# Kernel tuning notes

Hardware: AMD Instinct MI355X
Metric: run time of the kernel (lower is better)

The kernel has to match this reference:

```python
import jax, jax.numpy as jnp
import numpy as np

# --- Instant-NGP hash-grid constants (from __init__ defaults) ---
T = 2 ** 19          # hash table size per level
NLEVELS = 16
F = 2                # features per level
L = 4                # dir positional-encoding frequencies
LEVELS = np.geomspace(16, 2048, NLEVELS, dtype=int)            # grid resolutions
PRIMES = jnp.array([1, 2654435761, 805459861], dtype=jnp.uint32)
FREQS = (2.0 ** np.arange(L)).astype(np.float32)
# corner c in 0..7 -> bit b_i = use ceil along dim i (matches torch corner order)
BITS = jnp.array([[(c >> i) & 1 for i in range(3)] for c in range(8)], dtype=bool)  # (8,3)


def _hash_encode(pos, table):
    """pos: (P,3) level-scaled positions; table: (T,F). Returns (P,F).
    Spatial hash + gather + trilinear interpolation (== grid_sample trick)."""
    fl = jnp.floor(pos)
    ce = jnp.ceil(pos)
    frac = pos - fl                                             # (P,3) in [0,1)
    corners = jnp.where(BITS[None], ce[:, None, :], fl[:, None, :]).astype(jnp.int32)  # (P,8,3)
    # uint32 wrap-around arithmetic matches torch int64 mod 2^19 (T is a power of 2)
    v = corners.astype(jnp.uint32) * PRIMES                     # (P,8,3)
    h = (v[..., 0] ^ v[..., 1] ^ v[..., 2]) & jnp.uint32(T - 1) # (P,8)
    cf = table[h]                                               # (P,8,F) irregular gather
    w = jnp.prod(jnp.where(BITS[None], frac[:, None, :], 1.0 - frac[:, None, :]), axis=-1)  # (P,8)
    return jnp.einsum('pc,pcf->pf', w, cf)


def setup_inputs() -> dict:
    key = jax.random.key(0)
    ks = jax.random.split(key, 16)
    N, S = 2048, 192
    # positions s.t. x*scene_scale + 0.5 lies mostly in (0,1), a few outside (mask path)
    x = (jax.random.uniform(ks[0], (N, S, 3), jnp.float32) - 0.5) * 1.1
    r_dir = jax.random.normal(ks[1], (N, S, 3), jnp.float32)
    tables = jax.random.normal(ks[2], (NLEVELS, T, F), jnp.float32) * 1e-4

    def lin(k, fan_in, fan_out):
        return jax.random.normal(k, (fan_in, fan_out), jnp.float32) / np.float32(np.sqrt(fan_in))

    din = F * NLEVELS              # 32
    cin = 16 + 3 + 3 * L * 2       # 43
    return {
        'x': x, 'r_dir': r_dir, 'tables': tables,
        'dW1': lin(ks[3], din, 64), 'db1': jnp.zeros((64,), jnp.float32),
        'dW2': lin(ks[4], 64, 16), 'db2': jnp.zeros((16,), jnp.float32),
        'cW1': lin(ks[5], cin, 64), 'cb1': jnp.zeros((64,), jnp.float32),
        'cW2': lin(ks[6], 64, 64), 'cb2': jnp.zeros((64,), jnp.float32),
        'cW3': lin(ks[7], 64, 3), 'cb3': jnp.zeros((3,), jnp.float32),
    }


def reference(x, r_dir, tables, dW1, db1, dW2, db2, cW1, cb1, cW2, cb2, cW3, cb3):
    scene_scale = 1.0
    N, S = x.shape[0], r_dir.shape[1]
    xf = x.reshape(-1, 3) * scene_scale + 0.5          # (P,3)
    rd = r_dir.reshape(-1, 3)                          # (P,3)
    mask = jnp.all(xf > 0, axis=-1) & jnp.all(xf < 1, axis=-1)  # (P,)

    # multi-resolution hash encoding (fixed 16-level loop, vectorized over points)
    feats = jnp.concatenate(
        [_hash_encode(xf * np.float32(LEVELS[i]), tables[i]) for i in range(NLEVELS)],
        axis=-1)                                       # (P, F*NLEVELS)

    log_sigma = jax.nn.relu(feats @ dW1 + db1) @ dW2 + db2        # (P,16)

    # direction positional encoding: [dir, sin(2^l*2pi*dir), cos(...)] -> (P, 3+3*2L)
    xin = rd[..., None] * (2.0 * np.pi * jnp.asarray(FREQS))      # (P,3,L)
    enc = jnp.concatenate([jnp.sin(xin), jnp.cos(xin)], axis=-1).reshape(rd.shape[0], -1)
    enc_dir = jnp.concatenate([rd, enc], axis=-1)                 # (P,27)

    h = jax.nn.relu(jnp.concatenate([log_sigma, enc_dir], axis=-1) @ cW1 + cb1)
    h = jax.nn.relu(h @ cW2 + cb2)
    color = jax.nn.sigmoid(h @ cW3 + cb3)                         # (P,3)

    color = jnp.where(mask[:, None], color, 0.0)
    sigma = jnp.where(mask[:, None], jnp.exp(log_sigma[:, :1]), 0.0)
    return color.reshape(N, S, 3), sigma.reshape(N, S, 1)
```

## Files before the change

### kernel.cpp

```cpp
#include <hip/hip_runtime.h>
#include <hip/hip_bf16.h>
#include <cstdint>

#define NPTS (2048 * 192)
#define TBL  (1u << 19)
#define TMASK (TBL - 1u)
#define PBLOCKS (NPTS / 256)
#define ENC_BLOCKS (PBLOCKS * 16)
#define PREP_BLOCKS 6
#define PE_BLOCKS PBLOCKS
#define MLP_BLOCKS 3072
#define P2 2654435761u
#define P3 805459861u

__constant__ float LVLS[16] = {16.f, 22.f, 30.f, 42.f, 58.f, 80.f, 111.f, 153.f,
                               212.f, 294.f, 406.f, 561.f, 776.f, 1072.f, 1482.f, 2048.f};

__device__ __forceinline__ uint32_t f2bf(float f) {
    uint32_t u = __float_as_uint(f);
    return (u + 0x7FFFu + ((u >> 16) & 1u)) >> 16;
}
__device__ __forceinline__ uint32_t pack2(float a, float b) {
    return f2bf(a) | (f2bf(b) << 16);
}
__device__ __forceinline__ uint32_t pack2t(float a, float b) {
    return __builtin_amdgcn_perm(__float_as_uint(b), __float_as_uint(a),
                                 0x07060302u);
}

#if __has_builtin(__builtin_amdgcn_sinf)
#define SIN_REV(x) __builtin_amdgcn_sinf(x)
#else
#define SIN_REV(x) __sinf(6.28318530717958647f * (x))
#endif

typedef __attribute__((ext_vector_type(8))) short bf16x8;
typedef __attribute__((ext_vector_type(4))) float f32x4;

#define MFMA_BF16 __builtin_amdgcn_mfma_f32_16x16x32_bf16

__device__ __forceinline__ float pe_val(int r, float rx, float ry, float rz)
{
    int t = r - 19;
    int d = t >> 3;
    int s = t & 7;
    float comp = (d == 0) ? rx : ((d == 1) ? ry : rz);
    float a = ldexpf(comp, s & 3) + ((s >= 4) ? 0.25f : 0.0f);
    float v = SIN_REV(a);
    if (r == 16) v = rx;
    if (r == 17) v = ry;
    if (r == 18) v = rz;
    if (r == 43) v = 1.0f;
    if (r > 43)  v = 0.0f;
    return v;
}

__global__ __launch_bounds__(256) void k_encode(const float* __restrict__ x,
                                                const float* __restrict__ tables,
                                                uint32_t* __restrict__ feats,
                                                const float* __restrict__ dW1,
                                                const float* __restrict__ dW2,
                                                const float* __restrict__ cW1,
                                                const float* __restrict__ cb1,
                                                const float* __restrict__ cW2,
                                                const float* __restrict__ cW3,
                                                uint4* __restrict__ wfrags,
                                                const float* __restrict__ rdir,
                                                uint32_t* __restrict__ dirs)
{
    if (blockIdx.x >= ENC_BLOCKS + PREP_BLOCKS) {
        int p = (blockIdx.x - ENC_BLOCKS - PREP_BLOCKS) * 256 + threadIdx.x;
        size_t p3 = (size_t)p * 3;
        float rx = rdir[p3 + 0], ry = rdir[p3 + 1], rz = rdir[p3 + 2];
#pragma unroll
        for (int i = 0; i < 14; ++i)
            dirs[(size_t)i * NPTS + p] =
                pack2t(pe_val(16 + 2 * i, rx, ry, rz),
                       pe_val(17 + 2 * i, rx, ry, rz));
        return;
    }
    if (blockIdx.x >= ENC_BLOCKS) {
        int t = (blockIdx.x - ENC_BLOCKS) * 256 + threadIdx.x;
        if (t >= 24 * 64) return;
        int frag = t >> 6, lane = t & 63;
        const float* W; const float* bfold = nullptr;
        int OUT, Kact, Mact, k0, m0;
        if (frag < 4)       { W = dW1; OUT = 64; Kact = 32; Mact = 64; k0 = 0;               m0 = frag * 16; }
        else if (frag < 6)  { W = dW2; OUT = 16; Kact = 64; Mact = 16; k0 = (frag - 4) * 32; m0 = 0; }
        else if (frag < 14) { int i = frag - 6;  W = cW1; OUT = 64; Kact = 43; Mact = 64;
                              k0 = (i & 1) * 32; m0 = (i >> 1) * 16; bfold = cb1; }
        else if (frag < 22) { int i = frag - 14; W = cW2; OUT = 64; Kact = 64; Mact = 64;
                              k0 = (i & 1) * 32; m0 = (i >> 1) * 16; }
        else                { W = cW3; OUT = 3;  Kact = 64; Mact = 3;  k0 = (frag - 22) * 32; m0 = 0; }
        int m  = m0 + (lane & 15);
        int kq = k0 + ((lane >> 4) << 3);
        uint32_t d[4];
#pragma unroll
        for (int j = 0; j < 4; ++j) {
            float a0 = 0.f, a1 = 0.f;
            int ka = kq + 2 * j, kb = ka + 1;
            if (m < Mact) {
                a0 = (ka < Kact) ? W[(size_t)ka * OUT + m]
                                 : ((bfold && ka == Kact) ? bfold[m] : 0.f);
                a1 = (kb < Kact) ? W[(size_t)kb * OUT + m]
                                 : ((bfold && kb == Kact) ? bfold[m] : 0.f);
            }
            d[j] = f2bf(a0) | (f2bf(a1) << 16);
        }
        wfrags[t] = make_uint4(d[0], d[1], d[2], d[3]);
        return;
    }

    int xs   = blockIdx.x & 7;
    int i    = blockIdx.x >> 3;
    int half = i / PBLOCKS;
    int pb   = i - half * PBLOCKS;
    int lvl  = xs + (half << 3);
    int p    = pb * 256 + threadIdx.x;

    size_t p3 = (size_t)p * 3;
    float x0 = x[p3 + 0] + 0.5f;
    float x1 = x[p3 + 1] + 0.5f;
    float x2 = x[p3 + 2] + 0.5f;
    size_t oidx = (size_t)lvl * NPTS + p;

    bool m = (x0 > 0.f) && (x0 < 1.f) && (x1 > 0.f) && (x1 < 1.f) &&
             (x2 > 0.f) && (x2 < 1.f);
    if (!m) { feats[oidx] = 0u; return; }

    float s  = LVLS[lvl];
    float px = x0 * s, py = x1 * s, pz = x2 * s;
    float flx = floorf(px), fly = floorf(py), flz = floorf(pz);
    float frx = px - flx,   fry = py - fly,   frz = pz - flz;
    int ix = (int)flx, iy = (int)fly, iz = (int)flz;
    uint32_t ux = (uint32_t)ix, uy = (uint32_t)iy, uz = (uint32_t)iz;

    uint32_t base[4];
    base[0] = (uy * P2) ^ (uz * P3);
    base[1] = ((uy + 1u) * P2) ^ (uz * P3);
    base[2] = (uy * P2) ^ ((uz + 1u) * P3);
    base[3] = ((uy + 1u) * P2) ^ ((uz + 1u) * P3);

    const float2* tb = (const float2*)tables + (size_t)lvl * TBL;

    float2 v[8];
    if ((ix & 1) == 0) {
        const float4* tb4 = (const float4*)tb;
#pragma unroll
        for (int cc = 0; cc < 4; ++cc) {
            uint32_t h0 = (base[cc] ^ ux) & TMASK;
            float4 qv = tb4[h0 >> 1];
            bool hi = (h0 & 1u) != 0u;
            float2 e0 = hi ? make_float2(qv.z, qv.w) : make_float2(qv.x, qv.y);
            float2 e1 = hi ? make_float2(qv.x, qv.y) : make_float2(qv.z, qv.w);
            v[(cc << 1)]     = e0;
            v[(cc << 1) | 1] = e1;
        }
    } else {
        uint32_t h[8];
#pragma unroll
        for (int c = 0; c < 8; ++c)
            h[c] = (base[c >> 1] ^ (ux + (uint32_t)(c & 1))) & TMASK;
#pragma unroll
        for (int c = 0; c < 8; ++c) v[c] = tb[h[c]];
    }

    float f0 = 0.f, f1 = 0.f;
#pragma unroll
    for (int c = 0; c < 8; ++c) {
        float w = ((c & 1)        ? frx : 1.f - frx)
                * (((c >> 1) & 1) ? fry : 1.f - fry)
                * (((c >> 2) & 1) ? frz : 1.f - frz);
        f0 += w * v[c].x;
        f1 += w * v[c].y;
    }
    feats[oidx] = pack2(f0, f1);
}

__device__ __forceinline__ bf16x8 trans_frag(uint32_t p01a, uint32_t p23a,
                                             uint32_t p01b, uint32_t p23b, int lane)
{
    int q = lane >> 4, col = lane & 15;
    int srcA = (((q & 1) << 1) << 4) | col;
    int srcB = srcA + 16;
    uint32_t a0 = (uint32_t)__shfl((int)p01a, srcA, 64);
    uint32_t b0 = (uint32_t)__shfl((int)p01b, srcA, 64);
    uint32_t a1 = (uint32_t)__shfl((int)p23a, srcA, 64);
    uint32_t b1 = (uint32_t)__shfl((int)p23b, srcA, 64);
    uint32_t a2 = (uint32_t)__shfl((int)p01a, srcB, 64);
    uint32_t b2 = (uint32_t)__shfl((int)p01b, srcB, 64);
    uint32_t a3 = (uint32_t)__shfl((int)p23a, srcB, 64);
    uint32_t b3 = (uint32_t)__shfl((int)p23b, srcB, 64);
    bool hi = q >= 2;
    union { bf16x8 v; uint32_t d[4]; } u;
    u.d[0] = hi ? b0 : a0;
    u.d[1] = hi ? b1 : a1;
    u.d[2] = hi ? b2 : a2;
    u.d[3] = hi ? b3 : a3;
    return u.v;
}

__global__ __launch_bounds__(256, 4) void k_mlp(const uint32_t* __restrict__ feats,
                                                const uint4* __restrict__ wfrags,
                                                const float* __restrict__ x,
                                                const uint32_t* __restrict__ dirs,
                                                const float* __restrict__ db1,
                                                const float* __restrict__ db2,
                                                const float* __restrict__ cb2,
                                                const float* __restrict__ cb3,
                                                float* __restrict__ out)
{
    __shared__ uint4 wlds[24 * 64];
#pragma unroll
    for (int t = 0; t < 6; ++t)
        wlds[t * 256 + threadIdx.x] = wfrags[t * 256 + threadIdx.x];
    __syncthreads();

    int lane = threadIdx.x & 63;
    int q = lane >> 4, col = lane & 15;
    int wgid = blockIdx.x * 4 + (threadIdx.x >> 6);

#define LDW(f) ({ union { uint4 u_; bf16x8 v_; } w_; w_.u_ = wlds[(f) * 64 + lane]; w_.v_; })

#pragma unroll
    for (int it = 0; it < 2; ++it) {
        int g = (wgid * 2 + it) << 4;
        int pt = g + col;
        size_t pt3 = (size_t)pt * 3;

        union { bf16x8 v; uint32_t d[4]; } Bf;
#pragma unroll
        for (int w = 0; w < 4; ++w)
            Bf.d[w] = feats[(size_t)(q * 4 + w) * NPTS + g + col];

        uint32_t da[4], dbv[4];
#pragma unroll
        for (int j = 0; j < 4; ++j) {
            int pa = ((q - 2) * 4 + j) & 7;
            da[j] = dirs[(size_t)pa * NPTS + pt];
            int pb = 8 + q * 4 + j;
            pb = (pb > 13) ? 13 : pb;
            dbv[j] = dirs[(size_t)pb * NPTS + pt];
        }

        f32x4 T[4];
#pragma unroll
        for (int mt = 0; mt < 4; ++mt) {
            const float4 bb = *(const float4*)&db1[mt * 16 + q * 4];
            f32x4 c; c[0] = bb.x; c[1] = bb.y; c[2] = bb.z; c[3] = bb.w;
            T[mt] = MFMA_BF16(LDW(mt), Bf.v, c, 0, 0, 0);
        }
        uint32_t p01[4], p23[4];
#pragma unroll
        for (int mt = 0; mt < 4; ++mt) {
            p01[mt] = pack2t(fmaxf(T[mt][0], 0.f), fmaxf(T[mt][1], 0.f));
            p23[mt] = pack2t(fmaxf(T[mt][2], 0.f), fmaxf(T[mt][3], 0.f));
        }
        bf16x8 Bh0 = trans_frag(p01[0], p23[0], p01[1], p23[1], lane);
        bf16x8 Bh1 = trans_frag(p01[2], p23[2], p01[3], p23[3], lane);

        f32x4 Dls;
        {
            const float4 bb = *(const float4*)&db2[q * 4];
            f32x4 c; c[0] = bb.x; c[1] = bb.y; c[2] = bb.z; c[3] = bb.w;
            Dls = MFMA_BF16(LDW(4), Bh0, c, 0, 0, 0);
            Dls = MFMA_BF16(LDW(5), Bh1, Dls, 0, 0, 0);
        }
        uint32_t lp01 = pack2t(Dls[0], Dls[1]);
        uint32_t lp23 = pack2t(Dls[2], Dls[3]);

        union { bf16x8 v; uint32_t d[4]; } Ba0, Ba1;
        Ba0.v = trans_frag(lp01, lp23, lp01, lp23, lane);
#pragma unroll
        for (int j = 0; j < 4; ++j) {
            Ba0.d[j] = (q >= 2) ? da[j] : Ba0.d[j];
            bool vld = (q == 0) | ((q == 1) & (j < 2));
            Ba1.d[j] = vld ? dbv[j] : 0u;
        }

        f32x4 C1[4];
#pragma unroll
        for (int mt = 0; mt < 4; ++mt) {
            f32x4 c = {0.f, 0.f, 0.f, 0.f};
            c = MFMA_BF16(LDW(6 + 2 * mt), Ba0.v, c, 0, 0, 0);
            C1[mt] = MFMA_BF16(LDW(7 + 2 * mt), Ba1.v, c, 0, 0, 0);
        }
#pragma unroll
        for (int mt = 0; mt < 4; ++mt) {
            p01[mt] = pack2t(fmaxf(C1[mt][0], 0.f), fmaxf(C1[mt][1], 0.f));
            p23[mt] = pack2t(fmaxf(C1[mt][2], 0.f), fmaxf(C1[mt][3], 0.f));
        }
        bf16x8 Bc0 = trans_frag(p01[0], p23[0], p01[1], p23[1], lane);
        bf16x8 Bc1 = trans_frag(p01[2], p23[2], p01[3], p23[3], lane);

        f32x4 C2[4];
#pragma unroll
        for (int mt = 0; mt < 4; ++mt) {
            const float4 bb = *(const float4*)&cb2[mt * 16 + q * 4];
            f32x4 c; c[0] = bb.x; c[1] = bb.y; c[2] = bb.z; c[3] = bb.w;
            c = MFMA_BF16(LDW(14 + 2 * mt), Bc0, c, 0, 0, 0);
            C2[mt] = MFMA_BF16(LDW(15 + 2 * mt), Bc1, c, 0, 0, 0);
        }
#pragma unroll
        for (int mt = 0; mt < 4; ++mt) {
            p01[mt] = pack2t(fmaxf(C2[mt][0], 0.f), fmaxf(C2[mt][1], 0.f));
            p23[mt] = pack2t(fmaxf(C2[mt][2], 0.f), fmaxf(C2[mt][3], 0.f));
        }
        bf16x8 Bd0 = trans_frag(p01[0], p23[0], p01[1], p23[1], lane);
        bf16x8 Bd1 = trans_frag(p01[2], p23[2], p01[3], p23[3], lane);

        f32x4 c5 = {0.f, 0.f, 0.f, 0.f};
        if (q == 0) { c5[0] = cb3[0]; c5[1] = cb3[1]; c5[2] = cb3[2]; }
        f32x4 Dc = MFMA_BF16(LDW(22), Bd0, c5, 0, 0, 0);
        Dc = MFMA_BF16(LDW(23), Bd1, Dc, 0, 0, 0);

        if (q == 0) {
            float xfx = x[pt3 + 0] + 0.5f;
            float xfy = x[pt3 + 1] + 0.5f;
            float xfz = x[pt3 + 2] + 0.5f;
            bool m = (xfx > 0.f) && (xfx < 1.f) && (xfy > 0.f) && (xfy < 1.f) &&
                     (xfz > 0.f) && (xfz < 1.f);
            out[pt3 + 0] = m ? 1.f / (1.f + __expf(-Dc[0])) : 0.f;
            out[pt3 + 1] = m ? 1.f / (1.f + __expf(-Dc[1])) : 0.f;
            out[pt3 + 2] = m ? 1.f / (1.f + __expf(-Dc[2])) : 0.f;
            out[(size_t)3 * NPTS + pt] = m ? __expf(Dls[0]) : 0.f;
        }
    }
#undef LDW
}

extern "C" void kernel_launch(void* const* d_in, const int* in_sizes, int n_in,
                              void* d_out, int out_size, void* d_ws, size_t ws_size,
                              hipStream_t stream) {
    const float* x      = (const float*)d_in[0];
    const float* rdir   = (const float*)d_in[1];
    const float* tables = (const float*)d_in[2];
    const float* dW1 = (const float*)d_in[3];
    const float* db1 = (const float*)d_in[4];
    const float* dW2 = (const float*)d_in[5];
    const float* db2 = (const float*)d_in[6];
    const float* cW1 = (const float*)d_in[7];
    const float* cb1 = (const float*)d_in[8];
    const float* cW2 = (const float*)d_in[9];
    const float* cb2 = (const float*)d_in[10];
    const float* cW3 = (const float*)d_in[11];
    const float* cb3 = (const float*)d_in[12];
    float* out = (float*)d_out;

    uint4*    wfrags = (uint4*)d_ws;
    uint32_t* feats  = (uint32_t*)((char*)d_ws + 32768);
    uint32_t* dirs   = (uint32_t*)((char*)d_ws + 32768 + (size_t)16 * NPTS * 4);

    k_encode<<<ENC_BLOCKS + PREP_BLOCKS + PE_BLOCKS, 256, 0, stream>>>(
        x, tables, feats, dW1, dW2, cW1, cb1, cW2, cW3, wfrags, rdir, dirs);
    k_mlp<<<MLP_BLOCKS, 256, 0, stream>>>(feats, wfrags, x, dirs,
                                          db1, db2, cb2, cb3, out);
}
```

Baseline: 244.0 us.

## Split hash encode into two level-half launches, use permlane swaps, hoist MLP biases

The single encode launch becomes two: levels 0-7 plus the weight-fragment prep and direction encoding, then levels 8-15. The stated aim is to keep each half's hash-table working set more cache-friendly and to shrink the grid, at the cost of an extra launch. In the MLP, the 64-lane shuffle transposes are replaced with v_permlane32_swap/v_permlane16_swap sequences, which should avoid ds_bpermute traffic through LDS. Bias vectors are also loaded once before the loop instead of on every iteration, which raises register pressure.

```diff
diff --git a/kernel.cpp b/kernel.cpp
--- a/kernel.cpp
+++ b/kernel.cpp
@@ -6,7 +6,7 @@
 #define TBL  (1u << 19)
 #define TMASK (TBL - 1u)
 #define PBLOCKS (NPTS / 256)
-#define ENC_BLOCKS (PBLOCKS * 16)
+#define HALF_BLOCKS (PBLOCKS * 8)
 #define PREP_BLOCKS 6
 #define PE_BLOCKS PBLOCKS
 #define MLP_BLOCKS 3072
@@ -66,21 +66,23 @@
                                                 const float* __restrict__ cW3,
                                                 uint4* __restrict__ wfrags,
                                                 const float* __restrict__ rdir,
-                                                uint32_t* __restrict__ dirs)
-{
-    if (blockIdx.x >= ENC_BLOCKS + PREP_BLOCKS) {
-        int p = (blockIdx.x - ENC_BLOCKS - PREP_BLOCKS) * 256 + threadIdx.x;
-        size_t p3 = (size_t)p * 3;
-        float rx = rdir[p3 + 0], ry = rdir[p3 + 1], rz = rdir[p3 + 2];
-#pragma unroll
-        for (int i = 0; i < 14; ++i)
-            dirs[(size_t)i * NPTS + p] =
-                pack2t(pe_val(16 + 2 * i, rx, ry, rz),
-                       pe_val(17 + 2 * i, rx, ry, rz));
-        return;
-    }
-    if (blockIdx.x >= ENC_BLOCKS) {
-        int t = (blockIdx.x - ENC_BLOCKS) * 256 + threadIdx.x;
+                                                uint32_t* __restrict__ dirs,
+                                                int lvl_base)
+{
+    if (blockIdx.x >= HALF_BLOCKS) {
+        int tb = blockIdx.x - HALF_BLOCKS;
+        if (tb >= PREP_BLOCKS) {
+            int p = (tb - PREP_BLOCKS) * 256 + threadIdx.x;
+            size_t p3 = (size_t)p * 3;
+            float rx = rdir[p3 + 0], ry = rdir[p3 + 1], rz = rdir[p3 + 2];
+#pragma unroll
+            for (int i = 0; i < 14; ++i)
+                dirs[(size_t)i * NPTS + p] =
+                    pack2t(pe_val(16 + 2 * i, rx, ry, rz),
+                           pe_val(17 + 2 * i, rx, ry, rz));
+            return;
+        }
+        int t = tb * 256 + threadIdx.x;
         if (t >= 24 * 64) return;
         int frag = t >> 6, lane = t & 63;
         const float* W; const float* bfold = nullptr;
@@ -112,10 +114,8 @@
     }
 
     int xs   = blockIdx.x & 7;
-    int i    = blockIdx.x >> 3;
-    int half = i / PBLOCKS;
-    int pb   = i - half * PBLOCKS;
-    int lvl  = xs + (half << 3);
+    int pb   = blockIdx.x >> 3;
+    int lvl  = xs + lvl_base;
     int p    = pb * 256 + threadIdx.x;
 
     size_t p3 = (size_t)p * 3;
@@ -177,26 +177,40 @@
     feats[oidx] = pack2(f0, f1);
 }
 
+__device__ __forceinline__ void quad_gather(uint32_t x, uint32_t& e02, uint32_t& e13)
+{
+    uint32_t u = x, v = x;
+    asm("v_permlane32_swap_b32 %0, %1" : "+v"(u), "+v"(v));
+    asm("v_permlane16_swap_b32 %0, %1" : "+v"(u), "+v"(v));
+    e02 = u; e13 = v;
+}
+
 __device__ __forceinline__ bf16x8 trans_frag(uint32_t p01a, uint32_t p23a,
-                                             uint32_t p01b, uint32_t p23b, int lane)
-{
-    int q = lane >> 4, col = lane & 15;
-    int srcA = (((q & 1) << 1) << 4) | col;
-    int srcB = srcA + 16;
-    uint32_t a0 = (uint32_t)__shfl((int)p01a, srcA, 64);
-    uint32_t b0 = (uint32_t)__shfl((int)p01b, srcA, 64);
-    uint32_t a1 = (uint32_t)__shfl((int)p23a, srcA, 64);
-    uint32_t b1 = (uint32_t)__shfl((int)p23b, srcA, 64);
-    uint32_t a2 = (uint32_t)__shfl((int)p01a, srcB, 64);
-    uint32_t b2 = (uint32_t)__shfl((int)p01b, srcB, 64);
-    uint32_t a3 = (uint32_t)__shfl((int)p23a, srcB, 64);
-    uint32_t b3 = (uint32_t)__shfl((int)p23b, srcB, 64);
-    bool hi = q >= 2;
+                                             uint32_t p01b, uint32_t p23b, bool hi)
+{
+    uint32_t a02, a13, c02, c13, b02, b13, e02, e13;
+    quad_gather(p01a, a02, a13);
+    quad_gather(p23a, c02, c13);
+    quad_gather(p01b, b02, b13);
+    quad_gather(p23b, e02, e13);
     union { bf16x8 v; uint32_t d[4]; } u;
-    u.d[0] = hi ? b0 : a0;
-    u.d[1] = hi ? b1 : a1;
-    u.d[2] = hi ? b2 : a2;
-    u.d[3] = hi ? b3 : a3;
+    u.d[0] = hi ? b02 : a02;
+    u.d[1] = hi ? e02 : c02;
+    u.d[2] = hi ? b13 : a13;
+    u.d[3] = hi ? e13 : c13;
+    return u.v;
+}
+
+__device__ __forceinline__ bf16x8 trans_frag1(uint32_t p01, uint32_t p23)
+{
+    uint32_t a02, a13, c02, c13;
+    quad_gather(p01, a02, a13);
+    quad_gather(p23, c02, c13);
+    union { bf16x8 v; uint32_t d[4]; } u;
+    u.d[0] = a02;
+    u.d[1] = c02;
+    u.d[2] = a13;
+    u.d[3] = c13;
     return u.v;
 }
 
@@ -214,11 +228,22 @@
 #pragma unroll
     for (int t = 0; t < 6; ++t)
         wlds[t * 256 + threadIdx.x] = wfrags[t * 256 + threadIdx.x];
-    __syncthreads();
 
     int lane = threadIdx.x & 63;
     int q = lane >> 4, col = lane & 15;
+    bool hi = q >= 2;
     int wgid = blockIdx.x * 4 + (threadIdx.x >> 6);
+
+    float4 b1v[4], c2v[4];
+#pragma unroll
+    for (int mt = 0; mt < 4; ++mt) {
+        b1v[mt] = *(const float4*)&db1[mt * 16 + q * 4];
+        c2v[mt] = *(const float4*)&cb2[mt * 16 + q * 4];
+    }
+    float4 b2v = *(const float4*)&db2[q * 4];
+    float cb30 = cb3[0], cb31 = cb3[1], cb32 = cb3[2];
+
+    __syncthreads();
 
 #define LDW(f) ({ union { uint4 u_; bf16x8 v_; } w_; w_.u_ = wlds[(f) * 64 + lane]; w_.v_; })
 
@@ -246,8 +271,7 @@
         f32x4 T[4];
 #pragma unroll
         for (int mt = 0; mt < 4; ++mt) {
-            const float4 bb = *(const float4*)&db1[mt * 16 + q * 4];
-            f32x4 c; c[0] = bb.x; c[1] = bb.y; c[2] = bb.z; c[3] = bb.w;
+            f32x4 c; c[0] = b1v[mt].x; c[1] = b1v[mt].y; c[2] = b1v[mt].z; c[3] = b1v[mt].w;
             T[mt] = MFMA_BF16(LDW(mt), Bf.v, c, 0, 0, 0);
         }
         uint32_t p01[4], p23[4];
@@ -256,13 +280,12 @@
             p01[mt] = pack2t(fmaxf(T[mt][0], 0.f), fmaxf(T[mt][1], 0.f));
             p23[mt] = pack2t(fmaxf(T[mt][2], 0.f), fmaxf(T[mt][3], 0.f));
         }
-        bf16x8 Bh0 = trans_frag(p01[0], p23[0], p01[1], p23[1], lane);
-        bf16x8 Bh1 = trans_frag(p01[2], p23[2], p01[3], p23[3], lane);
+        bf16x8 Bh0 = trans_frag(p01[0], p23[0], p01[1], p23[1], hi);
+        bf16x8 Bh1 = trans_frag(p01[2], p23[2], p01[3], p23[3], hi);
 
         f32x4 Dls;
         {
-            const float4 bb = *(const float4*)&db2[q * 4];
-            f32x4 c; c[0] = bb.x; c[1] = bb.y; c[2] = bb.z; c[3] = bb.w;
+            f32x4 c; c[0] = b2v.x; c[1] = b2v.y; c[2] = b2v.z; c[3] = b2v.w;
             Dls = MFMA_BF16(LDW(4), Bh0, c, 0, 0, 0);
             Dls = MFMA_BF16(LDW(5), Bh1, Dls, 0, 0, 0);
         }
@@ -270,7 +293,7 @@
         uint32_t lp23 = pack2t(Dls[2], Dls[3]);
 
         union { bf16x8 v; uint32_t d[4]; } Ba0, Ba1;
-        Ba0.v = trans_frag(lp01, lp23, lp01, lp23, lane);
+        Ba0.v = trans_frag1(lp01, lp23);
 #pragma unroll
         for (int j = 0; j < 4; ++j) {
             Ba0.d[j] = (q >= 2) ? da[j] : Ba0.d[j];
@@ -290,14 +313,13 @@
             p01[mt] = pack2t(fmaxf(C1[mt][0], 0.f), fmaxf(C1[mt][1], 0.f));
             p23[mt] = pack2t(fmaxf(C1[mt][2], 0.f), fmaxf(C1[mt][3], 0.f));
         }
-        bf16x8 Bc0 = trans_frag(p01[0], p23[0], p01[1], p23[1], lane);
-        bf16x8 Bc1 = trans_frag(p01[2], p23[2], p01[3], p23[3], lane);
+        bf16x8 Bc0 = trans_frag(p01[0], p23[0], p01[1], p23[1], hi);
+        bf16x8 Bc1 = trans_frag(p01[2], p23[2], p01[3], p23[3], hi);
 
         f32x4 C2[4];
 #pragma unroll
         for (int mt = 0; mt < 4; ++mt) {
-            const float4 bb = *(const float4*)&cb2[mt * 16 + q * 4];
-            f32x4 c; c[0] = bb.x; c[1] = bb.y; c[2] = bb.z; c[3] = bb.w;
+            f32x4 c; c[0] = c2v[mt].x; c[1] = c2v[mt].y; c[2] = c2v[mt].z; c[3] = c2v[mt].w;
             c = MFMA_BF16(LDW(14 + 2 * mt), Bc0, c, 0, 0, 0);
             C2[mt] = MFMA_BF16(LDW(15 + 2 * mt), Bc1, c, 0, 0, 0);
         }
@@ -306,11 +328,11 @@
             p01[mt] = pack2t(fmaxf(C2[mt][0], 0.f), fmaxf(C2[mt][1], 0.f));
             p23[mt] = pack2t(fmaxf(C2[mt][2], 0.f), fmaxf(C2[mt][3], 0.f));
         }
-        bf16x8 Bd0 = trans_frag(p01[0], p23[0], p01[1], p23[1], lane);
-        bf16x8 Bd1 = trans_frag(p01[2], p23[2], p01[3], p23[3], lane);
+        bf16x8 Bd0 = trans_frag(p01[0], p23[0], p01[1], p23[1], hi);
+        bf16x8 Bd1 = trans_frag(p01[2], p23[2], p01[3], p23[3], hi);
 
         f32x4 c5 = {0.f, 0.f, 0.f, 0.f};
-        if (q == 0) { c5[0] = cb3[0]; c5[1] = cb3[1]; c5[2] = cb3[2]; }
+        if (q == 0) { c5[0] = cb30; c5[1] = cb31; c5[2] = cb32; }
         f32x4 Dc = MFMA_BF16(LDW(22), Bd0, c5, 0, 0, 0);
         Dc = MFMA_BF16(LDW(23), Bd1, Dc, 0, 0, 0);
 
@@ -351,8 +373,10 @@
     uint32_t* feats  = (uint32_t*)((char*)d_ws + 32768);
     uint32_t* dirs   = (uint32_t*)((char*)d_ws + 32768 + (size_t)16 * NPTS * 4);
 
-    k_encode<<<ENC_BLOCKS + PREP_BLOCKS + PE_BLOCKS, 256, 0, stream>>>(
-        x, tables, feats, dW1, dW2, cW1, cb1, cW2, cW3, wfrags, rdir, dirs);
+    k_encode<<<HALF_BLOCKS + PREP_BLOCKS + PE_BLOCKS, 256, 0, stream>>>(
+        x, tables, feats, dW1, dW2, cW1, cb1, cW2, cW3, wfrags, rdir, dirs, 0);
+    k_encode<<<HALF_BLOCKS, 256, 0, stream>>>(
+        x, tables, feats, dW1, dW2, cW1, cb1, cW2, cW3, wfrags, rdir, dirs, 8);
     k_mlp<<<MLP_BLOCKS, 256, 0, stream>>>(feats, wfrags, x, dirs,
                                           db1, db2, cb2, cb3, out);
 }
```

New measurement: 252.8 us. 1.04x slower.
